# Performance work log

Measured on AMD Instinct MI355X. Metric: run time of the kernel, lower is better.

Reference implementation:

```python
import jax, jax.numpy as jnp
import numpy as np

B, C, D, H, W = 1, 32, 48, 96, 192


def setup_inputs() -> dict:
    key = jax.random.key(0)
    ks = jax.random.split(key, 5)
    x = jax.random.normal(ks[0], (B, C, D, H, W), dtype=jnp.float32)
    gs = []
    for i in range(4):
        g = jax.random.uniform(ks[i + 1], (B, C, 5, H, W), dtype=jnp.float32)
        # GANet normalizes the 5 aggregation weights to sum to 1 per pixel
        g = g / jnp.sum(g, axis=2, keepdims=True)
        gs.append(g)
    return {"input": x, "g0": gs[0], "g1": gs[1], "g2": gs[2], "g3": gs[3]}


def _sga_dir(cost, g, axis, reverse):
    """Semi-global aggregation along one direction.

    cost: (B,C,D,H,W); g: (B,C,5,H,W). axis=4 scans along width, axis=3 along
    height; reverse flips the scan direction. Recurrence per step p:
      A(p,d) = w0*C(p,d) + w1*A(p-1,d) + w2*A(p-1,d-1) + w3*A(p-1,d+1)
               + w4*max_d' A(p-1,d')
    with A = C at the first position and d+-1 edge-clamped.
    """
    c = jnp.moveaxis(cost, axis, 0)  # (L, B, C, D, R)
    w = jnp.moveaxis(g, axis, 0)     # (L, B, C, 5, R)
    if reverse:
        c = c[::-1]
        w = w[::-1]

    def step(A, xs):
        cs, ws = xs  # cs: (B,C,D,R); ws: (B,C,5,R)
        w0, w1, w2, w3, w4 = (ws[:, :, k][:, :, None] for k in range(5))
        dm1 = jnp.concatenate([A[:, :, :1], A[:, :, :-1]], axis=2)  # d-1 (clamped)
        dp1 = jnp.concatenate([A[:, :, 1:], A[:, :, -1:]], axis=2)  # d+1 (clamped)
        mx = jnp.max(A, axis=2, keepdims=True)                      # max over d
        A_new = w0 * cs + w1 * A + w2 * dm1 + w3 * dp1 + w4 * mx
        return A_new, A_new

    A0 = c[0]
    _, outs = jax.lax.scan(step, A0, (c[1:], w[1:]))
    full = jnp.concatenate([A0[None], outs], axis=0)
    if reverse:
        full = full[::-1]
    return jnp.moveaxis(full, 0, axis)


def reference(input, g0, g1, g2, g3):
    a0 = _sga_dir(input, g0, 4, False)  # left -> right
    a1 = _sga_dir(input, g1, 4, True)   # right -> left
    a2 = _sga_dir(input, g2, 3, False)  # top -> bottom
    a3 = _sga_dir(input, g3, 3, True)   # bottom -> top
    # GANet selects the max over the 4 directions instead of summing
    return jnp.maximum(jnp.maximum(a0, a1), jnp.maximum(a2, a3))
```

## Files before the change

kernel.cpp:

```cpp
#include <hip/hip_runtime.h>

constexpr int Cc = 32;
constexpr int Dd = 48;
constexpr int Hh = 96;
constexpr int Ww = 192;
constexpr int TW = 16;
constexpr int NT = Ww / TW;
constexpr float NEGBIG = -3.402823466e+38f;

template <int CTRL, int RM>
__device__ __forceinline__ float dppmov(float v) {
    int i = __builtin_bit_cast(int, v);
    int r = __builtin_amdgcn_update_dpp(i, i, CTRL, RM, 0xF, false);
    return __builtin_bit_cast(float, r);
}

__device__ __forceinline__ float rdlane(float v, int idx) {
    int r = __builtin_amdgcn_readlane(__builtin_bit_cast(int, v), idx);
    return __builtin_bit_cast(float, r);
}

__device__ __forceinline__ unsigned f2h(float v) {
    return (unsigned)__builtin_bit_cast(unsigned short, (_Float16)v);
}
__device__ __forceinline__ float h2f(unsigned short u) {
    return (float)__builtin_bit_cast(_Float16, u);
}

__device__ __forceinline__ float wave_max48(float v) {
    v = fmaxf(v, dppmov<0x111, 0xF>(v));
    v = fmaxf(v, dppmov<0x112, 0xF>(v));
    v = fmaxf(v, dppmov<0x114, 0xF>(v));
    v = fmaxf(v, dppmov<0x118, 0xF>(v));
    v = fmaxf(v, dppmov<0x142, 0x2>(v));
    v = fmaxf(v, dppmov<0x143, 0x4>(v));
    return rdlane(v, 47);
}

__device__ __forceinline__ float sga_step(float A, float cs, float g0v, float g1v, float g2v,
                                          float g3v, float g4v, bool is47, bool first) {
    float dm1 = dppmov<0x138, 0xF>(A);
    float dp1 = dppmov<0x130, 0xF>(A);
    dp1 = is47 ? A : dp1;
    float mx = wave_max48(A);
    float r = g0v * cs + g1v * A + g2v * dm1 + g3v * dp1 + g4v * mx;
    return first ? cs : r;
}

template <bool DESC, bool STASH>
__device__ __forceinline__ void w6_run16(float& A, unsigned* tr, const unsigned* rr,
                                         float (*xo)[TW + 1], float gA, float g4r,
                                         int lane, int dl, bool is47, bool firstTile) {
#pragma unroll
    for (int k = 0; k < TW; ++k) {
        const int wk = DESC ? (TW - 1 - k) : k;
        const float g0v = rdlane(gA, wk);
        const float g1v = rdlane(gA, 16 + wk);
        const float g2v = rdlane(gA, 32 + wk);
        const float g3v = rdlane(gA, 48 + wk);
        const float g4v = rdlane(g4r, wk);
        const float cs = xo[dl][wk];
        A = sga_step(A, cs, g0v, g1v, g2v, g3v, g4v, is47, firstTile && (k == 0));
        if (STASH) {
            const unsigned hu = f2h(A);
            if (!DESC) {
                if ((wk & 1) == 0) tr[wk >> 1] = hu;
                else tr[wk >> 1] |= hu << 16;
            } else {
                if (wk & 1) tr[wk >> 1] = hu << 16;
                else tr[wk >> 1] |= hu;
            }
        } else {
            const unsigned u = rr[wk >> 1];
            const float aop = h2f((unsigned short)((wk & 1) ? (u >> 16) : (u & 0xffffu)));
            if (lane < Dd) xo[lane][wk] = fmaxf(A, aop);
        }
    }
}

__global__ __launch_bounds__(128, 4) void sga_w6(const float* __restrict__ x,
                                                 const float* __restrict__ ga,
                                                 const float* __restrict__ gb,
                                                 float* __restrict__ out) {
    __shared__ unsigned sstash[2][48][Dd];
    __shared__ float xo[2][Dd][TW + 1];

    const int bid = blockIdx.x;
    const int c = bid / Hh;
    const int h = bid - c * Hh;
    const int tid = threadIdx.x;
    const int lane = tid & 63;
    const int dir = tid >> 6;
    const size_t HW = (size_t)Hh * Ww;

    const float* xrow = x + (size_t)c * Dd * HW + (size_t)h * Ww;
    const float* grow = (dir ? gb : ga) + (size_t)c * 5 * HW + (size_t)h * Ww;
    float* orow = out + (size_t)c * Dd * HW + (size_t)h * Ww;

    const int dl = (lane < Dd) ? lane : (Dd - 1);
    const bool is47 = (lane == Dd - 1);

    int srow[3], scol[3];
#pragma unroll
    for (int i = 0; i < 3; ++i) {
        const int e4 = lane + i * 64;
        srow[i] = e4 >> 2;
        scol[i] = (e4 & 3) * 4;
    }
    const int gk = lane >> 4;
    const int gwi = lane & 15;

    float4 pre[3];
    float gA, g4r, gAn = 0.f, g4n = 0.f;
    unsigned tr[8];

    {
        const int t = dir ? (NT - 1) : 0;
        const int w0 = t * TW;
#pragma unroll
        for (int i = 0; i < 3; ++i)
            pre[i] = *reinterpret_cast<const float4*>(xrow + (size_t)srow[i] * HW + w0 + scol[i]);
        gA = grow[(size_t)gk * HW + w0 + gwi];
        g4r = grow[(size_t)4 * HW + w0 + gwi];
#pragma unroll
        for (int i = 0; i < 3; ++i) {
            xo[dir][srow[i]][scol[i] + 0] = pre[i].x;
            xo[dir][srow[i]][scol[i] + 1] = pre[i].y;
            xo[dir][srow[i]][scol[i] + 2] = pre[i].z;
            xo[dir][srow[i]][scol[i] + 3] = pre[i].w;
        }
    }

    float A = NEGBIG;

    for (int tt = 0; tt < NT; ++tt) {
        if (tt == NT / 2) __syncthreads();

        const int t = dir ? (NT - 1 - tt) : tt;
        const int w0 = t * TW;

        if (tt + 1 < NT) {
            const int wn = (dir ? (NT - 2 - tt) : (tt + 1)) * TW;
#pragma unroll
            for (int i = 0; i < 3; ++i)
                pre[i] = *reinterpret_cast<const float4*>(xrow + (size_t)srow[i] * HW + wn + scol[i]);
            gAn = grow[(size_t)gk * HW + wn + gwi];
            g4n = grow[(size_t)4 * HW + wn + gwi];
        }

        unsigned rr[8];
        if (tt >= NT / 2) {
#pragma unroll
            for (int r = 0; r < 8; ++r) rr[r] = sstash[dir ^ 1][(NT - 1 - tt) * 8 + r][dl];
        }

        if (tt < NT / 2) {
            if (dir == 0)
                w6_run16<false, true>(A, tr, rr, xo[0], gA, g4r, lane, dl, is47, tt == 0);
            else
                w6_run16<true, true>(A, tr, rr, xo[1], gA, g4r, lane, dl, is47, tt == 0);
            if (lane < Dd) {
#pragma unroll
                for (int r = 0; r < 8; ++r) sstash[dir][tt * 8 + r][lane] = tr[r];
            }
        } else {
            if (dir == 0)
                w6_run16<false, false>(A, tr, rr, xo[0], gA, g4r, lane, dl, is47, false);
            else
                w6_run16<true, false>(A, tr, rr, xo[1], gA, g4r, lane, dl, is47, false);
#pragma unroll
            for (int i = 0; i < 3; ++i) {
                float4 v;
                v.x = xo[dir][srow[i]][scol[i] + 0];
                v.y = xo[dir][srow[i]][scol[i] + 1];
                v.z = xo[dir][srow[i]][scol[i] + 2];
                v.w = xo[dir][srow[i]][scol[i] + 3];
                *reinterpret_cast<float4*>(orow + (size_t)srow[i] * HW + w0 + scol[i]) = v;
            }
        }

        if (tt + 1 < NT) {
#pragma unroll
            for (int i = 0; i < 3; ++i) {
                xo[dir][srow[i]][scol[i] + 0] = pre[i].x;
                xo[dir][srow[i]][scol[i] + 1] = pre[i].y;
                xo[dir][srow[i]][scol[i] + 2] = pre[i].z;
                xo[dir][srow[i]][scol[i] + 3] = pre[i].w;
            }
            gA = gAn;
            g4r = g4n;
        }
    }
}

constexpr int HWT = 8;
constexpr int HKH = 4;
constexpr int HNP = Hh / HKH;
constexpr int HHALF = HNP / 2;

__global__ __launch_bounds__(1024) void sga_h7(const float* __restrict__ x,
                                               const float* __restrict__ gf,
                                               const float* __restrict__ gr,
                                               float* __restrict__ out) {
    __shared__ _Float16 stash[HWT][2][Hh / 2][Dd];
    __shared__ float xs[2][2][HKH][Dd][9];
    __shared__ float osb[2][2][HKH][Dd][9];
    __shared__ float gs[2][2][HKH][HWT][8];

    const int xcd = blockIdx.x & 7;
    const int within = blockIdx.x >> 3;
    const int pairid = xcd * 48 + (within >> 1);
    const int sub = within & 1;
    const int c = pairid / 12;
    const int w0 = ((pairid % 12) * 2 + sub) * HWT;

    const int tid = threadIdx.x;
    const int lane = tid & 63;
    const int wv = tid >> 6;
    const int col = wv >> 1;
    const int dir = wv & 1;
    const size_t HW = (size_t)Hh * Ww;

    const float* xb = x + (size_t)c * Dd * HW;
    const float* gfb = gf + (size_t)c * 5 * HW;
    const float* grb = gr + (size_t)c * 5 * HW;
    float* ob = out + (size_t)c * Dd * HW;

    const int dl = (lane < Dd) ? lane : (Dd - 1);
    const bool is47 = (lane == Dd - 1);

    int w_[3], d_[3], hp_[3], cu_[3];
    size_t xoff_[3];
#pragma unroll
    for (int j = 0; j < 3; ++j) {
        const int idx = tid + j * 1024;
        w_[j] = idx & 7;
        const int t = idx >> 3;
        d_[j] = t % Dd;
        const int t2 = t / Dd;
        hp_[j] = t2 & 3;
        cu_[j] = t2 >> 2;
        xoff_[j] = (size_t)d_[j] * HW + (w0 + w_[j]);
    }
    const int gw_ = tid & 7;
    const int gk_ = (tid >> 3) % 5;
    const int ghc = (tid >> 3) / 5;
    const int ghp_ = ghc & 3;
    const int gcu_ = ghc >> 2;
    const bool gst = tid < 320;

    auto hofs = [&](int cur, int P, int hp) -> int {
        const int p = P * HKH + hp;
        return cur ? (Hh - 1 - p) : p;
    };

    float xr_[3], grg = 0.f, orr[2][3];

    {
#pragma unroll
        for (int j = 0; j < 3; ++j) xr_[j] = xb[xoff_[j] + (size_t)hofs(cu_[j], 0, hp_[j]) * Ww];
        if (gst) {
            const float* gp = gcu_ ? grb : gfb;
            grg = gp[(size_t)gk_ * HW + (size_t)hofs(gcu_, 0, ghp_) * Ww + (w0 + gw_)];
        }
#pragma unroll
        for (int j = 0; j < 3; ++j) xs[0][cu_[j]][hp_[j]][d_[j]][w_[j]] = xr_[j];
        if (gst) gs[0][gcu_][ghp_][gw_][gk_] = grg;
    }
    __syncthreads();

    float A = NEGBIG;

#pragma unroll 2
    for (int p = 0; p < HNP; ++p) {
        const int pb = p & 1;

        if (p + 1 < HNP) {
#pragma unroll
            for (int j = 0; j < 3; ++j)
                xr_[j] = xb[xoff_[j] + (size_t)hofs(cu_[j], p + 1, hp_[j]) * Ww];
            if (gst) {
                const float* gp = gcu_ ? grb : gfb;
                grg = gp[(size_t)gk_ * HW + (size_t)hofs(gcu_, p + 1, ghp_) * Ww + (w0 + gw_)];
            }
        }
        if (p >= HHALF) {
#pragma unroll
            for (int j = 0; j < 3; ++j)
                orr[pb][j] = ob[xoff_[j] + (size_t)hofs(cu_[j], p, hp_[j]) * Ww];
        }

#pragma unroll
        for (int hp = 0; hp < HKH; ++hp) {
            const int q = p * HKH + hp;
            const float cs = xs[pb][dir][hp][dl][col];
            const float* gbase = &gs[pb][dir][hp][col][0];
            const float4 g03 = *reinterpret_cast<const float4*>(gbase);
            const float g4 = gbase[4];
            A = sga_step(A, cs, g03.x, g03.y, g03.z, g03.w, g4, is47, q == 0);
            if (q < Hh / 2) {
                if (lane < Dd) stash[col][dir][q][lane] = (_Float16)A;
            } else {
                const float s = (float)stash[col][dir ^ 1][Hh - 1 - q][dl];
                const float o = fmaxf(A, s);
                if (lane < Dd) osb[pb][dir][hp][lane][col] = o;
            }
        }

        if (p > HHALF) {
#pragma unroll
            for (int j = 0; j < 3; ++j) {
                const float v = fmaxf(osb[pb ^ 1][cu_[j]][hp_[j]][d_[j]][w_[j]], orr[pb ^ 1][j]);
                ob[xoff_[j] + (size_t)hofs(cu_[j], p - 1, hp_[j]) * Ww] = v;
            }
        }

        if (p + 1 < HNP) {
#pragma unroll
            for (int j = 0; j < 3; ++j) xs[pb ^ 1][cu_[j]][hp_[j]][d_[j]][w_[j]] = xr_[j];
            if (gst) gs[pb ^ 1][gcu_][ghp_][gw_][gk_] = grg;
        }
        __syncthreads();
    }

    {
#pragma unroll
        for (int j = 0; j < 3; ++j) {
            const float v = fmaxf(osb[1][cu_[j]][hp_[j]][d_[j]][w_[j]], orr[1][j]);
            ob[xoff_[j] + (size_t)hofs(cu_[j], HNP - 1, hp_[j]) * Ww] = v;
        }
    }
}

extern "C" void kernel_launch(void* const* d_in, const int* in_sizes, int n_in,
                              void* d_out, int out_size, void* d_ws, size_t ws_size,
                              hipStream_t stream) {
    const float* x  = (const float*)d_in[0];
    const float* g0 = (const float*)d_in[1];
    const float* g1 = (const float*)d_in[2];
    const float* g2 = (const float*)d_in[3];
    const float* g3 = (const float*)d_in[4];
    float* out = (float*)d_out;

    sga_w6<<<Cc * Hh, 128, 0, stream>>>(x, g0, g1, out);
    sga_h7<<<Cc * (Ww / HWT), 1024, 0, stream>>>(x, g2, g3, out);
}
```

Baseline: 250.4 us.

## Reorder kernels: H pass writes fp16 workspace, W pass fuses final max

When a large enough workspace is available, the vertical pass now runs first. It writes its combined result as packed fp16 into a tiled workspace instead of doing a read-modify-write of the fp32 output. The horizontal pass then reads that workspace and applies the final max before its single output store. This removes one full fp32 read and write of the output tensor in exchange for a half-size intermediate write and read, with fp16 rounding on the vertical-pass values.

```diff
diff --git a/kernel.cpp b/kernel.cpp
--- a/kernel.cpp
+++ b/kernel.cpp
@@ -7,6 +7,8 @@
 constexpr int TW = 16;
 constexpr int NT = Ww / TW;
 constexpr float NEGBIG = -3.402823466e+38f;
+
+constexpr size_t WSNEED = (size_t)Cc * 24 * Hh * 192 * 4;
 
 template <int CTRL, int RM>
 __device__ __forceinline__ float dppmov(float v) {
@@ -78,10 +80,12 @@
     }
 }
 
+template <bool WS>
 __global__ __launch_bounds__(128, 4) void sga_w6(const float* __restrict__ x,
                                                  const float* __restrict__ ga,
                                                  const float* __restrict__ gb,
-                                                 float* __restrict__ out) {
+                                                 float* __restrict__ out,
+                                                 const unsigned* __restrict__ ws) {
     __shared__ unsigned sstash[2][48][Dd];
     __shared__ float xo[2][Dd][TW + 1];
 
@@ -149,9 +153,21 @@
         }
 
         unsigned rr[8];
+        unsigned wsv[6];
         if (tt >= NT / 2) {
 #pragma unroll
             for (int r = 0; r < 8; ++r) rr[r] = sstash[dir ^ 1][(NT - 1 - tt) * 8 + r][dl];
+            if constexpr (WS) {
+#pragma unroll
+                for (int i = 0; i < 3; ++i) {
+                    const int wb = (w0 + scol[i]) >> 3;
+                    const int wi = scol[i] & 7;
+                    const size_t base =
+                        (((size_t)c * 24 + wb) * Hh + h) * 192 + srow[i] * 4 + (wi >> 1);
+                    wsv[2 * i] = ws[base];
+                    wsv[2 * i + 1] = ws[base + 1];
+                }
+            }
         }
 
         if (tt < NT / 2) {
@@ -175,6 +191,12 @@
                 v.y = xo[dir][srow[i]][scol[i] + 1];
                 v.z = xo[dir][srow[i]][scol[i] + 2];
                 v.w = xo[dir][srow[i]][scol[i] + 3];
+                if constexpr (WS) {
+                    v.x = fmaxf(v.x, h2f((unsigned short)(wsv[2 * i] & 0xffffu)));
+                    v.y = fmaxf(v.y, h2f((unsigned short)(wsv[2 * i] >> 16)));
+                    v.z = fmaxf(v.z, h2f((unsigned short)(wsv[2 * i + 1] & 0xffffu)));
+                    v.w = fmaxf(v.w, h2f((unsigned short)(wsv[2 * i + 1] >> 16)));
+                }
                 *reinterpret_cast<float4*>(orow + (size_t)srow[i] * HW + w0 + scol[i]) = v;
             }
         }
@@ -198,10 +220,12 @@
 constexpr int HNP = Hh / HKH;
 constexpr int HHALF = HNP / 2;
 
-__global__ __launch_bounds__(1024) void sga_h7(const float* __restrict__ x,
+template <bool WS>
+__global__ __launch_bounds__(1024) void sga_h9(const float* __restrict__ x,
                                                const float* __restrict__ gf,
                                                const float* __restrict__ gr,
-                                               float* __restrict__ out) {
+                                               float* __restrict__ out,
+                                               unsigned* __restrict__ ws) {
     __shared__ _Float16 stash[HWT][2][Hh / 2][Dd];
     __shared__ float xs[2][2][HKH][Dd][9];
     __shared__ float osb[2][2][HKH][Dd][9];
@@ -248,6 +272,21 @@
     const int ghp_ = ghc & 3;
     const int gcu_ = ghc >> 2;
     const bool gst = tid < 320;
+    int fu_[2], fd_[2], fhp_[2], fcu_[2];
+    bool fval_[2];
+#pragma unroll
+    for (int j = 0; j < 2; ++j) {
+        int idx = tid + j * 1024;
+        fval_[j] = idx < 1536;
+        if (idx >= 1536) idx = 1535;
+        fu_[j] = idx & 3;
+        const int t = idx >> 2;
+        fd_[j] = t % Dd;
+        const int r = t / Dd;
+        fhp_[j] = r & 3;
+        fcu_[j] = r >> 2;
+    }
+    const size_t wsblk = ((size_t)c * 24 + (w0 >> 3)) * Hh;
 
     auto hofs = [&](int cur, int P, int hp) -> int {
         const int p = P * HKH + hp;
@@ -284,10 +323,12 @@
                 grg = gp[(size_t)gk_ * HW + (size_t)hofs(gcu_, p + 1, ghp_) * Ww + (w0 + gw_)];
             }
         }
-        if (p >= HHALF) {
-#pragma unroll
-            for (int j = 0; j < 3; ++j)
-                orr[pb][j] = ob[xoff_[j] + (size_t)hofs(cu_[j], p, hp_[j]) * Ww];
+        if constexpr (!WS) {
+            if (p >= HHALF) {
+#pragma unroll
+                for (int j = 0; j < 3; ++j)
+                    orr[pb][j] = ob[xoff_[j] + (size_t)hofs(cu_[j], p, hp_[j]) * Ww];
+            }
         }
 
 #pragma unroll
@@ -308,10 +349,24 @@
         }
 
         if (p > HHALF) {
-#pragma unroll
-            for (int j = 0; j < 3; ++j) {
-                const float v = fmaxf(osb[pb ^ 1][cu_[j]][hp_[j]][d_[j]][w_[j]], orr[pb ^ 1][j]);
-                ob[xoff_[j] + (size_t)hofs(cu_[j], p - 1, hp_[j]) * Ww] = v;
+            if constexpr (WS) {
+#pragma unroll
+                for (int j = 0; j < 2; ++j) {
+                    if (fval_[j]) {
+                        const float* orow = &osb[pb ^ 1][fcu_[j]][fhp_[j]][fd_[j]][0];
+                        const unsigned pk =
+                            f2h(orow[2 * fu_[j]]) | (f2h(orow[2 * fu_[j] + 1]) << 16);
+                        const int hh = hofs(fcu_[j], p - 1, fhp_[j]);
+                        ws[(wsblk + hh) * 192 + fd_[j] * 4 + fu_[j]] = pk;
+                    }
+                }
+            } else {
+#pragma unroll
+                for (int j = 0; j < 3; ++j) {
+                    const float v = fmaxf(osb[pb ^ 1][cu_[j]][hp_[j]][d_[j]][w_[j]],
+                                          orr[pb ^ 1][j]);
+                    ob[xoff_[j] + (size_t)hofs(cu_[j], p - 1, hp_[j]) * Ww] = v;
+                }
             }
         }
 
@@ -323,7 +378,17 @@
         __syncthreads();
     }
 
-    {
+    if constexpr (WS) {
+#pragma unroll
+        for (int j = 0; j < 2; ++j) {
+            if (fval_[j]) {
+                const float* orow = &osb[1][fcu_[j]][fhp_[j]][fd_[j]][0];
+                const unsigned pk = f2h(orow[2 * fu_[j]]) | (f2h(orow[2 * fu_[j] + 1]) << 16);
+                const int hh = hofs(fcu_[j], HNP - 1, fhp_[j]);
+                ws[(wsblk + hh) * 192 + fd_[j] * 4 + fu_[j]] = pk;
+            }
+        }
+    } else {
 #pragma unroll
         for (int j = 0; j < 3; ++j) {
             const float v = fmaxf(osb[1][cu_[j]][hp_[j]][d_[j]][w_[j]], orr[1][j]);
@@ -342,6 +407,11 @@
     const float* g3 = (const float*)d_in[4];
     float* out = (float*)d_out;
 
-    sga_w6<<<Cc * Hh, 128, 0, stream>>>(x, g0, g1, out);
-    sga_h7<<<Cc * (Ww / HWT), 1024, 0, stream>>>(x, g2, g3, out);
-}
+    if (ws_size >= WSNEED) {
+        sga_h9<true><<<Cc * (Ww / HWT), 1024, 0, stream>>>(x, g2, g3, out, (unsigned*)d_ws);
+        sga_w6<true><<<Cc * Hh, 128, 0, stream>>>(x, g0, g1, out, (const unsigned*)d_ws);
+    } else {
+        sga_w6<false><<<Cc * Hh, 128, 0, stream>>>(x, g0, g1, out, nullptr);
+        sga_h9<false><<<Cc * (Ww / HWT), 1024, 0, stream>>>(x, g2, g3, out, nullptr);
+    }
+}
```

Result: faster. 240.4 us (-4.0%).
